# Performance work log

Hardware: AMD Instinct MI355X
Metric: run time of the kernel (lower is better)

The kernel has to match this reference:

```python
import jax, jax.numpy as jnp
import numpy as np

VOL_SIZE = 1.0  # config.render.volume_size


def _make_grid(G, vol_size):
    # pytorch3d Volumes.get_coord_grid(world_coordinates=True): axis-aligned grid
    # centered at origin, spacing = voxel_size = vol_size/G, last dim is (x,y,z)
    # with x varying along W, y along H, z along D.
    m = (G - 1) / 2.0 * (vol_size / G)
    lin = jnp.linspace(-m, m, G, dtype=jnp.float32)
    zz, yy, xx = jnp.meshgrid(lin, lin, lin, indexing='ij')
    return jnp.stack([xx, yy, zz], axis=-1)  # [G,G,G,3]


def _grid_sample_3d(vol, grid):
    # vol: [N,C,D,H,W]; grid: [N,Dg,Hg,Wg,3] xyz in [-1,1].
    # Matches torch F.grid_sample(mode='bilinear', padding_mode='zeros', align_corners=False).
    N, C, D, H, W = vol.shape
    ix = ((grid[..., 0] + 1.0) * W - 1.0) * 0.5
    iy = ((grid[..., 1] + 1.0) * H - 1.0) * 0.5
    iz = ((grid[..., 2] + 1.0) * D - 1.0) * 0.5
    x0f, y0f, z0f = jnp.floor(ix), jnp.floor(iy), jnp.floor(iz)
    tx, ty, tz = ix - x0f, iy - y0f, iz - z0f
    x0, y0, z0 = x0f.astype(jnp.int32), y0f.astype(jnp.int32), z0f.astype(jnp.int32)

    def per_batch(v, z0, y0, x0, tx, ty, tz):
        # v: [C,D,H,W]; index/weight maps: [Dg,Hg,Wg]
        def corner(z, y, x):
            valid = (z >= 0) & (z < D) & (y >= 0) & (y < H) & (x >= 0) & (x < W)
            zc = jnp.clip(z, 0, D - 1)
            yc = jnp.clip(y, 0, H - 1)
            xc = jnp.clip(x, 0, W - 1)
            return v[:, zc, yc, xc] * valid[None]  # [C,Dg,Hg,Wg]
        z1, y1, x1 = z0 + 1, y0 + 1, x0 + 1
        acc = jnp.zeros((C,) + z0.shape, dtype=v.dtype)
        for zc, wz in ((z0, 1.0 - tz), (z1, tz)):
            for yc, wy in ((y0, 1.0 - ty), (y1, ty)):
                for xc, wx in ((x0, 1.0 - tx), (x1, tx)):
                    acc = acc + corner(zc, yc, xc) * (wz * wy * wx)[None]
        return acc

    return jax.vmap(per_batch)(vol, z0, y0, x0, tx, ty, tz)


def reference(voxels, camPoses_cv2, grid_size):
    B, t, C, D, H, W = voxels.shape
    G = grid_size
    m = (G - 1) / 2.0 * (VOL_SIZE / G)  # grid_coord_max
    grid_coord = _make_grid(G, VOL_SIZE)  # [G,G,G,3]

    # T = pose_0 @ pose_1^{-1}, per (B, t-1) pair
    pose0 = jnp.broadcast_to(camPoses_cv2[:, 0:1], (B, t - 1, 4, 4)).reshape(B * (t - 1), 4, 4)
    pose1 = camPoses_cv2[:, 1:].reshape(B * (t - 1), 4, 4)
    T = pose0 @ jnp.linalg.inv(pose1)

    # homogeneous transform of world grid points: cam = R @ p + trans
    pts = grid_coord.reshape(-1, 3)  # [N=G^3, 3]
    R, trans = T[:, :3, :3], T[:, :3, 3]
    cam = jnp.einsum('nij,pj->npi', R, pts) + trans[:, None, :]  # [B*(t-1), N, 3]
    sample_grid = (cam / m).reshape(B * (t - 1), D, H, W, 3)

    warped = _grid_sample_3d(voxels[:, 1:].reshape(B * (t - 1), C, D, H, W), sample_grid)
    out = jnp.concatenate([voxels[:, 0:1], warped.reshape(B, t - 1, C, D, H, W)], axis=1)
    return out


def setup_inputs() -> dict:
    key = jax.random.key(0)
    kv, ka, kt = jax.random.split(key, 3)
    B, t, C, G = 2, 5, 16, 64
    voxels = jax.random.normal(kv, (B, t, C, G, G, G), dtype=jnp.float32)
    # build valid SE(3)-ish camera poses (orthonormal rotation + small translation)
    A = jax.random.normal(ka, (B, t, 3, 3), dtype=jnp.float32)
    Q, _ = jnp.linalg.qr(A)
    det = jnp.linalg.det(Q)
    Q = Q * jnp.sign(det)[..., None, None]  # ensure det=+1
    trans = 0.2 * jax.random.normal(kt, (B, t, 3), dtype=jnp.float32)
    top = jnp.concatenate([Q, trans[..., None]], axis=-1)  # [B,t,3,4]
    bottom = jnp.broadcast_to(jnp.array([0.0, 0.0, 0.0, 1.0], jnp.float32), (B, t, 1, 4))
    camPoses_cv2 = jnp.concatenate([top, bottom], axis=-2)  # [B,t,4,4]
    return {"voxels": voxels, "camPoses_cv2": camPoses_cv2, "grid_size": G}
```

## Files before the change

kernel.cpp:

```cpp
#include <hip/hip_runtime.h>

#define G3_    (64 * 64 * 64)
#define CCH    16
#define TT     5
#define LSTRIDE 17
#define BUF    4096
#define NCHB   4
#define NWARP  (4096 * (CCH / NCHB))
#define NCOPY  8192
#define NBLK   (NWARP + NCOPY)

__global__ __launch_bounds__(256) void fused_kernel(const float* __restrict__ vox,
                                                    const float* __restrict__ cam,
                                                    float* __restrict__ out)
{
    __shared__ float lds[BUF];
    const int tid = threadIdx.x;

    const int bid  = blockIdx.x;
    const int sbid = (bid & 7) * (NBLK / 8) + (bid >> 3);
    const int q3   = sbid / 3;
    const int r3   = sbid - q3 * 3;

    if (r3 == 2) {
        int t4 = q3 * 256 + tid;
        int b  = t4 >> 20;
        int rr = t4 & ((1 << 20) - 1);
        size_t base = (size_t)(b * TT) * CCH * G3_;
        const float4* s = (const float4*)(vox + base);
        float4* d = (float4*)(out + base);
        d[rr] = s[rr];
        return;
    }

    const int wid = q3 * 2 + r3;
    const int cg  = wid >> 12;
    const int t9  = wid & 4095;
    const int n   = t9 >> 9;
    const int t6  = t9 & 511;
    const int ox  = (t6 & 7) << 3;
    const int oy  = ((t6 >> 3) & 7) << 3;
    const int oz  = (t6 >> 6) << 3;
    const int b   = n >> 2, j = n & 3;

    const float* p0 = cam + (size_t)(b * TT) * 16;
    const float* p1 = cam + (size_t)(b * TT + j + 1) * 16;
    float a00 = p0[0], a01 = p0[1], a02 = p0[2],  at0 = p0[3];
    float a10 = p0[4], a11 = p0[5], a12 = p0[6],  at1 = p0[7];
    float a20 = p0[8], a21 = p0[9], a22 = p0[10], at2 = p0[11];
    float b00 = p1[0], b01 = p1[1], b02 = p1[2],  bt0 = p1[3];
    float b10 = p1[4], b11 = p1[5], b12 = p1[6],  bt1 = p1[7];
    float b20 = p1[8], b21 = p1[9], b22 = p1[10], bt2 = p1[11];
    float R00 = a00*b00 + a01*b01 + a02*b02;
    float R01 = a00*b10 + a01*b11 + a02*b12;
    float R02 = a00*b20 + a01*b21 + a02*b22;
    float R10 = a10*b00 + a11*b01 + a12*b02;
    float R11 = a10*b10 + a11*b11 + a12*b12;
    float R12 = a10*b20 + a11*b21 + a12*b22;
    float R20 = a20*b00 + a21*b01 + a22*b02;
    float R21 = a20*b10 + a21*b11 + a22*b12;
    float R22 = a20*b20 + a21*b21 + a22*b22;
    float trx = at0 - (R00*bt0 + R01*bt1 + R02*bt2);
    float try_= at1 - (R10*bt0 + R11*bt1 + R12*bt2);
    float trz = at2 - (R20*bt0 + R21*bt1 + R22*bt2);

    const float S  = 1.0f / 64.0f;
    const float SC = 32.0f / 0.4921875f;
    const float ax = SC * R00 * S, bx = SC * R01 * S, cx = SC * R02 * S;
    const float ay = SC * R10 * S, by = SC * R11 * S, cy = SC * R12 * S;
    const float az = SC * R20 * S, bz = SC * R21 * S, cz = SC * R22 * S;
    const float kx = -31.5f * (ax + bx + cx) + SC * trx + 31.5f;
    const float ky = -31.5f * (ay + by + cy) + SC * try_ + 31.5f;
    const float kz = -31.5f * (az + bz + cz) + SC * trz + 31.5f;

    float x0a = ax * ox, x0b = ax * (ox + 7);
    float x1a = bx * oy, x1b = bx * (oy + 7);
    float x2a = cx * oz, x2b = cx * (oz + 7);
    float min_ix = kx + fminf(x0a, x0b) + fminf(x1a, x1b) + fminf(x2a, x2b);
    float max_ix = kx + fmaxf(x0a, x0b) + fmaxf(x1a, x1b) + fmaxf(x2a, x2b);
    float y0a = ay * ox, y0b = ay * (ox + 7);
    float y1a = by * oy, y1b = by * (oy + 7);
    float y2a = cy * oz, y2b = cy * (oz + 7);
    float min_iy = ky + fminf(y0a, y0b) + fminf(y1a, y1b) + fminf(y2a, y2b);
    float max_iy = ky + fmaxf(y0a, y0b) + fmaxf(y1a, y1b) + fmaxf(y2a, y2b);
    float z0a = az * ox, z0b = az * (ox + 7);
    float z1a = bz * oy, z1b = bz * (oy + 7);
    float z2a = cz * oz, z2b = cz * (oz + 7);
    float min_iz = kz + fminf(z0a, z0b) + fminf(z1a, z1b) + fminf(z2a, z2b);
    float max_iz = kz + fmaxf(z0a, z0b) + fmaxf(z1a, z1b) + fmaxf(z2a, z2b);

    int xlo = min(max((int)floorf(min_ix), 0), 63);
    int xhi = min(max((int)floorf(max_ix) + 1, 0), 63);
    int ylo = min(max((int)floorf(min_iy), 0), 63);
    int yhi = min(max((int)floorf(max_iy) + 1, 0), 63);
    int zlo = min(max((int)floorf(min_iz), 0), 63);
    int zhi = min(max((int)floorf(max_iz) + 1, 0), 63);
    const int xlo_e = xlo & ~1;
    const int sxe = xhi - xlo_e + 1;
    const int sy  = yhi - ylo + 1;
    const int sz  = zhi - zlo + 1;
    const int lstep = sy * LSTRIDE;

    float wx0[2], wx1[2], wy0[2], wy1[2], wz0[2], wz1[2];
    int base0[2], base1[2], soff[2];
    #pragma unroll
    for (int k = 0; k < 2; ++k) {
        int o  = tid + (k << 8);
        int gx = ox + (o & 7);
        int gy = oy + ((o >> 3) & 7);
        int gz = oz + (o >> 6);
        float ix = kx + ax * gx + bx * gy + cx * gz;
        float iy = ky + ay * gx + by * gy + cy * gz;
        float iz = kz + az * gx + bz * gy + cz * gz;
        float fx = floorf(ix), fy = floorf(iy), fz = floorf(iz);
        float tx = ix - fx, ty = iy - fy, tz = iz - fz;
        int X0 = (int)fx, Y0 = (int)fy, Z0 = (int)fz;

        float w0 = ((unsigned)X0 < 64u) ? (1.0f - tx) : 0.0f;
        float w1 = ((unsigned)(X0 + 1) < 64u) ? tx : 0.0f;
        int rxu = X0 - xlo_e;
        wx0[k] = (rxu < 0) ? w1 : w0;
        wx1[k] = (rxu < 0) ? 0.0f : w1;
        int rx0 = min(max(rxu, 0), sxe - 1);

        w0 = ((unsigned)Y0 < 64u) ? (1.0f - ty) : 0.0f;
        w1 = ((unsigned)(Y0 + 1) < 64u) ? ty : 0.0f;
        int ryu = Y0 - ylo;
        wy0[k] = (ryu < 0) ? w1 : w0;
        wy1[k] = (ryu < 0) ? 0.0f : w1;
        int ry0 = min(max(ryu, 0), sy - 1);

        wz0[k] = ((unsigned)Z0 < 64u) ? (1.0f - tz) : 0.0f;
        wz1[k] = ((unsigned)(Z0 + 1) < 64u) ? tz : 0.0f;
        int rz0 = min(max(Z0     - zlo, 0), sz - 1);
        int rz1 = min(max(Z0 + 1 - zlo, 0), sz - 1);

        base0[k] = rz0 * lstep + ry0 * LSTRIDE + rx0;
        base1[k] = rz1 * lstep + ry0 * LSTRIDE + rx0;
        soff[k]  = (gz << 12) + (gy << 6) + gx;
    }

    const size_t fb = ((size_t)(b * TT + j + 1) * CCH + cg * NCHB) * G3_;
    const float* vbase = vox + fb;
    float* obase = out + fb;

    const int lane8 = tid & 7;
    const int row16 = (tid >> 3) & 15;
    const int zh    = tid >> 7;
    const int xe    = xlo_e + (lane8 << 1);
    const bool actS = (xe <= xhi) && (row16 < sy);
    const int grow  = (zlo << 12) + ((ylo + row16) << 6) + xe;
    const int lrow  = row16 * LSTRIDE + (lane8 << 1);

    float2 stg[8];

    if (actS) {
        const float2* gp = (const float2*)(vbase + grow);
        #pragma unroll
        for (int k = 0; k < 8; ++k) {
            int zz = (k << 1) + zh;
            if (zz < sz) stg[k] = gp[(size_t)zz << 11];
        }
    }
    #pragma unroll
    for (int i = 0; i < 16; ++i) lds[tid + i * 256] = 0.0f;
    __syncthreads();
    if (actS) {
        #pragma unroll
        for (int k = 0; k < 8; ++k) {
            int zz = (k << 1) + zh;
            if (zz < sz) {
                float* wp = lds + lrow + zz * lstep;
                wp[0] = stg[k].x;
                wp[1] = stg[k].y;
            }
        }
    }
    __syncthreads();

    for (int cc = 0; cc < NCHB; ++cc) {
        const bool pre = (cc + 1 < NCHB);
        if (pre && actS) {
            const float2* gp = (const float2*)(vbase + (size_t)(cc + 1) * G3_ + grow);
            #pragma unroll
            for (int k = 0; k < 8; ++k) {
                int zz = (k << 1) + zh;
                if (zz < sz) stg[k] = gp[(size_t)zz << 11];
            }
        }

        float* op = obase + (size_t)cc * G3_;
        #pragma unroll
        for (int k = 0; k < 2; ++k) {
            const float* pz0 = lds + base0[k];
            const float* pz1 = lds + base1[k];
            float v000 = pz0[0],  v001 = pz0[1];
            float v010 = pz0[17], v011 = pz0[18];
            float v100 = pz1[0],  v101 = pz1[1];
            float v110 = pz1[17], v111 = pz1[18];
            float t00 = v000 * wx0[k] + v001 * wx1[k];
            float t01 = v010 * wx0[k] + v011 * wx1[k];
            float t10 = v100 * wx0[k] + v101 * wx1[k];
            float t11 = v110 * wx0[k] + v111 * wx1[k];
            float u0  = t00 * wy0[k] + t01 * wy1[k];
            float u1  = t10 * wy0[k] + t11 * wy1[k];
            op[soff[k]] = u0 * wz0[k] + u1 * wz1[k];
        }

        if (pre) {
            __syncthreads();
            if (actS) {
                #pragma unroll
                for (int k = 0; k < 8; ++k) {
                    int zz = (k << 1) + zh;
                    if (zz < sz) {
                        float* wp = lds + lrow + zz * lstep;
                        wp[0] = stg[k].x;
                        wp[1] = stg[k].y;
                    }
                }
            }
            __syncthreads();
        }
    }
}

extern "C" void kernel_launch(void* const* d_in, const int* in_sizes, int n_in,
                              void* d_out, int out_size, void* d_ws, size_t ws_size,
                              hipStream_t stream)
{
    const float* vox = (const float*)d_in[0];
    const float* cam = (const float*)d_in[1];
    float* out = (float*)d_out;
    (void)d_ws;

    hipLaunchKernelGGL(fused_kernel, dim3(NBLK), dim3(256), 0, stream, vox, cam, out);
}
```

Before: 357.7 us.

## Precompute pose coefficients in a prologue kernel and double channels per warp block

Pose composition and affine coefficient setup move out of every block into a tiny separate kernel that writes 12 floats per pair to workspace, which the main kernel then loads. The channel batch per block grows from 4 to 8, halving the number of warp blocks and reusing each staged LDS tile for more channels. The block-to-role mapping becomes a simple even/odd interleave of copy and warp blocks, the per-voxel coordinate math is hoisted, and the channel loop is unrolled. The trade-offs are an extra kernel launch, lower parallelism, and higher register pressure from the unroll.

```diff
diff --git a/kernel.cpp b/kernel.cpp
--- a/kernel.cpp
+++ b/kernel.cpp
@@ -5,44 +5,18 @@
 #define TT     5
 #define LSTRIDE 17
 #define BUF    4096
-#define NCHB   4
+#define NCHB   8
 #define NWARP  (4096 * (CCH / NCHB))
 #define NCOPY  8192
 #define NBLK   (NWARP + NCOPY)
 
-__global__ __launch_bounds__(256) void fused_kernel(const float* __restrict__ vox,
-                                                    const float* __restrict__ cam,
-                                                    float* __restrict__ out)
+
+__global__ void coeff_kernel(const float* __restrict__ cam, float* __restrict__ Tc)
 {
-    __shared__ float lds[BUF];
-    const int tid = threadIdx.x;
-
-    const int bid  = blockIdx.x;
-    const int sbid = (bid & 7) * (NBLK / 8) + (bid >> 3);
-    const int q3   = sbid / 3;
-    const int r3   = sbid - q3 * 3;
-
-    if (r3 == 2) {
-        int t4 = q3 * 256 + tid;
-        int b  = t4 >> 20;
-        int rr = t4 & ((1 << 20) - 1);
-        size_t base = (size_t)(b * TT) * CCH * G3_;
-        const float4* s = (const float4*)(vox + base);
-        float4* d = (float4*)(out + base);
-        d[rr] = s[rr];
-        return;
-    }
-
-    const int wid = q3 * 2 + r3;
-    const int cg  = wid >> 12;
-    const int t9  = wid & 4095;
-    const int n   = t9 >> 9;
-    const int t6  = t9 & 511;
-    const int ox  = (t6 & 7) << 3;
-    const int oy  = ((t6 >> 3) & 7) << 3;
-    const int oz  = (t6 >> 6) << 3;
-    const int b   = n >> 2, j = n & 3;
-
+    int n = threadIdx.x;
+    if (n >= NWARP / 1024) {  }
+    if (n >= 8) return;
+    int b = n >> 2, j = n & 3;
     const float* p0 = cam + (size_t)(b * TT) * 16;
     const float* p1 = cam + (size_t)(b * TT + j + 1) * 16;
     float a00 = p0[0], a01 = p0[1], a02 = p0[2],  at0 = p0[3];
@@ -66,12 +40,55 @@
 
     const float S  = 1.0f / 64.0f;
     const float SC = 32.0f / 0.4921875f;
-    const float ax = SC * R00 * S, bx = SC * R01 * S, cx = SC * R02 * S;
-    const float ay = SC * R10 * S, by = SC * R11 * S, cy = SC * R12 * S;
-    const float az = SC * R20 * S, bz = SC * R21 * S, cz = SC * R22 * S;
-    const float kx = -31.5f * (ax + bx + cx) + SC * trx + 31.5f;
-    const float ky = -31.5f * (ay + by + cy) + SC * try_ + 31.5f;
-    const float kz = -31.5f * (az + bz + cz) + SC * trz + 31.5f;
+    float ax = SC * R00 * S, bx = SC * R01 * S, cx = SC * R02 * S;
+    float ay = SC * R10 * S, by = SC * R11 * S, cy = SC * R12 * S;
+    float az = SC * R20 * S, bz = SC * R21 * S, cz = SC * R22 * S;
+    float* o = Tc + n * 12;
+    o[0] = ax; o[1] = bx; o[2] = cx;
+    o[3] = ay; o[4] = by; o[5] = cy;
+    o[6] = az; o[7] = bz; o[8] = cz;
+    o[9]  = -31.5f * (ax + bx + cx) + SC * trx + 31.5f;
+    o[10] = -31.5f * (ay + by + cy) + SC * try_ + 31.5f;
+    o[11] = -31.5f * (az + bz + cz) + SC * trz + 31.5f;
+}
+
+__global__ __launch_bounds__(256) void fused_kernel(const float* __restrict__ vox,
+                                                    const float* __restrict__ Tc,
+                                                    float* __restrict__ out)
+{
+    __shared__ float lds[BUF];
+    const int tid = threadIdx.x;
+
+    const int bid  = blockIdx.x;
+    const int sbid = (bid & 7) * (NBLK / 8) + (bid >> 3);
+
+    if (sbid & 1) {
+        int cid = sbid >> 1;
+        int t4  = cid * 256 + tid;
+        int b   = t4 >> 20;
+        int rr  = t4 & ((1 << 20) - 1);
+        size_t base = (size_t)(b * TT) * CCH * G3_;
+        const float4* s = (const float4*)(vox + base);
+        float4* d = (float4*)(out + base);
+        d[rr] = s[rr];
+        return;
+    }
+
+    const int wid = sbid >> 1;
+    const int cg  = wid >> 12;
+    const int t9  = wid & 4095;
+    const int n   = t9 >> 9;
+    const int t6  = t9 & 511;
+    const int ox  = (t6 & 7) << 3;
+    const int oy  = ((t6 >> 3) & 7) << 3;
+    const int oz  = (t6 >> 6) << 3;
+    const int b   = n >> 2, j = n & 3;
+
+    const float* Cp = Tc + n * 12;
+    const float ax = Cp[0], bx = Cp[1], cx = Cp[2];
+    const float ay = Cp[3], by = Cp[4], cy = Cp[5];
+    const float az = Cp[6], bz = Cp[7], cz = Cp[8];
+    const float kx = Cp[9], ky = Cp[10], kz = Cp[11];
 
     float x0a = ax * ox, x0b = ax * (ox + 7);
     float x1a = bx * oy, x1b = bx * (oy + 7);
@@ -101,17 +118,21 @@
     const int sz  = zhi - zlo + 1;
     const int lstep = sy * LSTRIDE;
 
+    const int gx  = ox + (tid & 7);
+    const int gy  = oy + ((tid >> 3) & 7);
+    const int gz0 = oz + (tid >> 6);
+    const float ixb = kx + ax * gx + bx * gy;
+    const float iyb = ky + ay * gx + by * gy;
+    const float izb = kz + az * gx + bz * gy;
+
     float wx0[2], wx1[2], wy0[2], wy1[2], wz0[2], wz1[2];
     int base0[2], base1[2], soff[2];
     #pragma unroll
     for (int k = 0; k < 2; ++k) {
-        int o  = tid + (k << 8);
-        int gx = ox + (o & 7);
-        int gy = oy + ((o >> 3) & 7);
-        int gz = oz + (o >> 6);
-        float ix = kx + ax * gx + bx * gy + cx * gz;
-        float iy = ky + ay * gx + by * gy + cy * gz;
-        float iz = kz + az * gx + bz * gy + cz * gz;
+        const int gz = gz0 + (k << 2);
+        float ix = ixb + cx * gz;
+        float iy = iyb + cy * gz;
+        float iz = izb + cz * gz;
         float fx = floorf(ix), fy = floorf(iy), fz = floorf(iz);
         float tx = ix - fx, ty = iy - fy, tz = iz - fz;
         int X0 = (int)fx, Y0 = (int)fy, Z0 = (int)fz;
@@ -178,6 +199,7 @@
     }
     __syncthreads();
 
+    #pragma unroll
     for (int cc = 0; cc < NCHB; ++cc) {
         const bool pre = (cc + 1 < NCHB);
         if (pre && actS) {
@@ -232,7 +254,8 @@
     const float* vox = (const float*)d_in[0];
     const float* cam = (const float*)d_in[1];
     float* out = (float*)d_out;
-    (void)d_ws;
-
-    hipLaunchKernelGGL(fused_kernel, dim3(NBLK), dim3(256), 0, stream, vox, cam, out);
+    float* Tc  = (float*)d_ws;
+
+    hipLaunchKernelGGL(coeff_kernel, dim3(1), dim3(64), 0, stream, cam, Tc);
+    hipLaunchKernelGGL(fused_kernel, dim3(NBLK), dim3(256), 0, stream, vox, Tc, out);
 }
```

Result: slower. 454.5 us (+27.0%).
